# Kernel tuning notes

Hardware: AMD Instinct MI355X
Metric: run time of the kernel (lower is better)

## Reference

```python
import jax, jax.numpy as jnp
import numpy as np
from jax import lax


def setup_inputs() -> dict:
    key = jax.random.key(0)
    kx, kw = jax.random.split(key)
    x = jax.random.normal(kx, (32, 3, 8192), dtype=jnp.float32)
    weight = jax.random.normal(kw, (128, 3, 64), dtype=jnp.float32)
    return {"x": x, "weight": weight}


def reference(x, weight):
    # x: [B, C, L], weight: [O, C, K]
    K = weight.shape[2]
    # Cross-correlation (conv1d, no bias, valid padding): [B, O, L-K+1]
    conv_out = lax.conv_general_dilated(
        x, weight, window_strides=(1,), padding='VALID',
        dimension_numbers=('NCH', 'OIH', 'NCH'))
    # Half squared norm of each shapelet: [O]
    w_norm = jnp.sum(weight ** 2, axis=(1, 2)) / 2
    # Half squared norm of each length-K window, via cumulative sums
    # (avoids materializing the [B, C, W, K] unfold tensor)
    sq = jnp.sum(x ** 2, axis=1)               # [B, L]
    c = jnp.pad(jnp.cumsum(sq, axis=1), ((0, 0), (1, 0)))  # [B, L+1]
    win_norm = (c[:, K:] - c[:, :-K]) / 2      # [B, L-K+1]
    # features = conv_out - (||w||^2/2 + ||window||^2/2)
    features = conv_out - w_norm[None, :, None] - win_norm[:, None, :]
    # global max-pool over time, then *(-2) -> min squared distance
    return -2.0 * jnp.max(features, axis=-1)   # [B, O]
```

## Files before the change

kernel.cpp:

```cpp
#include <hip/hip_runtime.h>
#include <hip/hip_bf16.h>
#include <float.h>

#define BB 32
#define LL 8192
#define OO 128
#define KK 64
#define WW (LL - KK + 1)
#define NCH 3
#define GX 11

typedef __attribute__((ext_vector_type(8))) short short8;
typedef __attribute__((ext_vector_type(4))) float f32x4;

union AB { int4 i4; int i[4]; short8 v; };

static __device__ __forceinline__ unsigned int pkbf(float a, float b) {
    union { __hip_bfloat162 h; unsigned int u; } cv;
    cv.h = __float22bfloat162_rn(make_float2(a, b));
    return cv.u;
}

__global__ __launch_bounds__(256) void prep_kernel(const float* __restrict__ w,
                                                   unsigned short* __restrict__ wswz,
                                                   float* __restrict__ wn,
                                                   float* __restrict__ out) {
    int g = blockIdx.x * 256 + threadIdx.x;
    if (g < 3072) {
        int ob = g / 768;
        int rem = g - ob * 768;
        int rr = rem >> 5, o2 = rem & 31;
        int ks = rr >> 2, qp = rr & 3;
        int c = ks >> 1, h = ks & 1;
        const float* p = w + (size_t)(ob * 32 + o2) * 192 + c * 64 + h * 32 + qp * 8;
        float4 v0 = *(const float4*)p, v1 = *(const float4*)(p + 4);
        int4 pk;
        pk.x = (int)pkbf(v0.x, v0.y);
        pk.y = (int)pkbf(v0.z, v0.w);
        pk.z = (int)pkbf(v1.x, v1.y);
        pk.w = (int)pkbf(v1.z, v1.w);
        ((int4*)wswz)[g] = pk;
    }
    int oo = g - 3072;
    if (oo >= 0 && oo < OO) {
        const float* p = w + oo * 192;
        float s = 0.f;
        for (int i = 0; i < 192; ++i) { float v = p[i]; s = fmaf(v, v, s); }
        wn[oo] = 0.5f * s;
    }
    int oi = g - 3200;
    if (oi >= 0 && oi < BB * OO) out[oi] = 3.389e38f;
}

static __device__ __forceinline__ void stage_load(const float* __restrict__ x, int b, int T0,
                                                  int tid, float4* v) {
    v[0] = make_float4(0.f, 0.f, 0.f, 0.f);
    v[1] = v[0];
    v[2] = v[0];
    if (tid < 80) {
        int l = T0 + 4 * tid;
        if (l < LL) {
            const float* p = x + (size_t)b * 3 * LL + l;
            v[0] = *(const float4*)(p);
            v[1] = *(const float4*)(p + LL);
            v[2] = *(const float4*)(p + 2 * LL);
        }
    }
}

static __device__ __forceinline__ void stage_store(int tid, const float4* v,
                                                   unsigned short* xl, float* sql, float* Pl) {
    if (tid >= 80) return;
    #pragma unroll
    for (int c = 0; c < 3; ++c) {
        uint2 pk;
        pk.x = pkbf(v[c].x, v[c].y);
        pk.y = pkbf(v[c].z, v[c].w);
        *(uint2*)(xl + c * 320 + tid * 4) = pk;
    }
    float4 sq4;
    sq4.x = fmaf(v[2].x, v[2].x, fmaf(v[1].x, v[1].x, v[0].x * v[0].x));
    sq4.y = fmaf(v[2].y, v[2].y, fmaf(v[1].y, v[1].y, v[0].y * v[0].y));
    sq4.z = fmaf(v[2].z, v[2].z, fmaf(v[1].z, v[1].z, v[0].z * v[0].z));
    sq4.w = fmaf(v[2].w, v[2].w, fmaf(v[1].w, v[1].w, v[0].w * v[0].w));
    *(float4*)(sql + tid * 4) = sq4;
    float s4 = (sq4.x + sq4.y) + (sq4.z + sq4.w);
    float s8 = s4 + __shfl_xor(s4, 1, 64);
    if ((tid & 1) == 0) Pl[tid >> 1] = s8;
}

__global__ __launch_bounds__(256, 4) void shapeconv_main(const float* __restrict__ x,
                                                         const unsigned short* __restrict__ wswz,
                                                         const float* __restrict__ wn,
                                                         float* __restrict__ out) {
    __shared__ __align__(16) unsigned short w_lds[6144];
    __shared__ __align__(16) unsigned short x_lds[2][3 * 320];
    __shared__ __align__(16) float sq_lds[2][320];
    __shared__ __align__(16) float P_lds[2][40];
    __shared__ float wn_lds[32];
    __shared__ float mred[32];

    const int tcx = blockIdx.x;
    const int ob = blockIdx.y;
    const int b  = blockIdx.z;
    const int tid = threadIdx.x;
    const int wv = tid >> 6;
    const int lane = tid & 63;
    const int wo = wv & 1, wt = wv >> 1;
    const int n  = lane & 15;
    const int qp = lane >> 4;
    const int Tb = tcx * (NCH * 256);
    const int rem = (WW - Tb + 255) >> 8;
    const int nch_eff = rem < NCH ? rem : NCH;

    {
        const char* src = (const char*)wswz + (size_t)ob * 12288 + tid * 16;
        #pragma unroll
        for (int i = 0; i < 3; ++i) {
            __builtin_amdgcn_global_load_lds(
                (const __attribute__((address_space(1))) unsigned int*)(src + i * 4096),
                (__attribute__((address_space(3))) unsigned int*)((char*)w_lds + tid * 16 + i * 4096),
                16, 0, 0);
        }
    }
    if (tid < 32) wn_lds[tid] = wn[ob * 32 + tid];

    float4 sv[3];
    stage_load(x, b, Tb, tid, sv);
    stage_store(tid, sv, x_lds[0], sq_lds[0], P_lds[0]);
    __syncthreads();

    float nw4[4];
    #pragma unroll
    for (int rg = 0; rg < 4; ++rg) nw4[rg] = wn_lds[16 * wo + 4 * qp + rg];

    float m2[4];
    #pragma unroll
    for (int rg = 0; rg < 4; ++rg) m2[rg] = -FLT_MAX;

    for (int ci = 0; ci < nch_eff; ++ci) {
        const int bsel = ci & 1;
        const int T0 = Tb + ci * 256;
        const bool more = (ci + 1 < nch_eff);
        if (more) stage_load(x, b, T0 + 256, tid, sv);

        float wl[8];
        {
            const float* sqp = sq_lds[bsel];
            const float* Pl  = P_lds[bsel];
            const int mi = 16 * wt + n;
            float S = 0.f;
            #pragma unroll
            for (int i = 0; i < 8; ++i) S += Pl[mi + i];
            #pragma unroll
            for (int r = 0; r < 8; ++r) {
                wl[r] = (T0 + 8 * mi + r < WW) ? 0.5f * S : 1e30f;
                if (r < 7) S += sqp[8 * mi + 64 + r] - sqp[8 * mi + r];
            }
        }

        f32x4 acc[8];
        #pragma unroll
        for (int r = 0; r < 8; ++r)
            #pragma unroll
            for (int rg = 0; rg < 4; ++rg)
                acc[r][rg] = -nw4[rg] - wl[r];

        const char* xb = (const char*)x_lds[bsel];
        __builtin_amdgcn_s_setprio(1);
        #pragma unroll
        for (int ks = 0; ks < 6; ++ks) {
            int c = ks >> 1, h = ks & 1;
            int e0b = c * 640 + 256 * wt + 64 * h + 16 * (n + qp);
            int4 Ea = *(const int4*)(xb + e0b);
            int4 Eb = *(const int4*)(xb + e0b + 16);
            int D[8] = {Ea.x, Ea.y, Ea.z, Ea.w, Eb.x, Eb.y, Eb.z, Eb.w};
            AB a0;
            a0.i4 = ((const int4*)w_lds)[(ks * 4 + qp) * 32 + 16 * wo + n];
            #pragma unroll
            for (int r = 0; r < 8; ++r) {
                AB bf;
                int s = r >> 1;
                if ((r & 1) == 0) {
                    bf.i[0] = D[s]; bf.i[1] = D[s + 1]; bf.i[2] = D[s + 2]; bf.i[3] = D[s + 3];
                } else {
                    #pragma unroll
                    for (int d = 0; d < 4; ++d)
                        bf.i[d] = (int)__builtin_amdgcn_alignbit((unsigned)D[s + d + 1],
                                                                 (unsigned)D[s + d], 16);
                }
                acc[r] = __builtin_amdgcn_mfma_f32_16x16x32_bf16(a0.v, bf.v, acc[r], 0, 0, 0);
            }
        }
        __builtin_amdgcn_s_setprio(0);

        #pragma unroll
        for (int rg = 0; rg < 4; ++rg) {
            float mm = m2[rg];
            #pragma unroll
            for (int r = 0; r < 8; ++r) mm = fmaxf(mm, acc[r][rg]);
            m2[rg] = mm;
        }

        if (more) {
            stage_store(tid, sv, x_lds[1 - bsel], sq_lds[1 - bsel], P_lds[1 - bsel]);
            __syncthreads();
        }
    }

    #pragma unroll
    for (int s = 1; s <= 8; s <<= 1)
        #pragma unroll
        for (int rg = 0; rg < 4; ++rg)
            m2[rg] = fmaxf(m2[rg], __shfl_xor(m2[rg], s, 64));

    if (wt == 1 && n == 0) {
        #pragma unroll
        for (int rg = 0; rg < 4; ++rg)
            mred[16 * wo + 4 * qp + rg] = m2[rg];
    }
    __syncthreads();
    if (wt == 0 && n == 0) {
        #pragma unroll
        for (int rg = 0; rg < 4; ++rg) {
            int oi = 16 * wo + 4 * qp + rg;
            float v = fmaxf(m2[rg], mred[oi]);
            atomicMin((int*)(out + (size_t)b * OO + ob * 32 + oi),
                      __float_as_int(-2.0f * v));
        }
    }
}

extern "C" void kernel_launch(void* const* d_in, const int* in_sizes, int n_in,
                              void* d_out, int out_size, void* d_ws, size_t ws_size,
                              hipStream_t stream) {
    const float* x = (const float*)d_in[0];
    const float* w = (const float*)d_in[1];
    float* out = (float*)d_out;

    unsigned short* wswz = (unsigned short*)d_ws;
    float* wn = (float*)((char*)d_ws + 49152);

    prep_kernel<<<29, 256, 0, stream>>>(w, wswz, wn, out);
    dim3 grid(GX, 4, BB);
    shapeconv_main<<<grid, 256, 0, stream>>>(x, wswz, wn, out);
}
```

Before: 77.07 us.

## Give each wave a private 128-sample time tile covering all 32 outputs, no chunk loop

Each wave now owns its own 128-position time tile and computes both 16-output halves of the block's 32 outputs. Before, the 4 waves split outputs and time inside a shared 256-sample chunk, and each block looped over 3 double-buffered chunks. The grid grows to 16 time blocks, and each block loads its x tile once into per-wave LDS. This removes the chunk loop, the cross-wave LDS reduction and most barriers. The cost is more atomics to global memory (one per wave per output), redundant loading of the overlapping 64-sample halo, and more accumulator registers per wave.

```diff
diff --git a/kernel.cpp b/kernel.cpp
--- a/kernel.cpp
+++ b/kernel.cpp
@@ -7,8 +7,7 @@
 #define OO 128
 #define KK 64
 #define WW (LL - KK + 1)
-#define NCH 3
-#define GX 11
+#define TCX 16
 
 typedef __attribute__((ext_vector_type(8))) short short8;
 typedef __attribute__((ext_vector_type(4))) float f32x4;
@@ -52,53 +51,14 @@
     if (oi >= 0 && oi < BB * OO) out[oi] = 3.389e38f;
 }
 
-static __device__ __forceinline__ void stage_load(const float* __restrict__ x, int b, int T0,
-                                                  int tid, float4* v) {
-    v[0] = make_float4(0.f, 0.f, 0.f, 0.f);
-    v[1] = v[0];
-    v[2] = v[0];
-    if (tid < 80) {
-        int l = T0 + 4 * tid;
-        if (l < LL) {
-            const float* p = x + (size_t)b * 3 * LL + l;
-            v[0] = *(const float4*)(p);
-            v[1] = *(const float4*)(p + LL);
-            v[2] = *(const float4*)(p + 2 * LL);
-        }
-    }
-}
-
-static __device__ __forceinline__ void stage_store(int tid, const float4* v,
-                                                   unsigned short* xl, float* sql, float* Pl) {
-    if (tid >= 80) return;
-    #pragma unroll
-    for (int c = 0; c < 3; ++c) {
-        uint2 pk;
-        pk.x = pkbf(v[c].x, v[c].y);
-        pk.y = pkbf(v[c].z, v[c].w);
-        *(uint2*)(xl + c * 320 + tid * 4) = pk;
-    }
-    float4 sq4;
-    sq4.x = fmaf(v[2].x, v[2].x, fmaf(v[1].x, v[1].x, v[0].x * v[0].x));
-    sq4.y = fmaf(v[2].y, v[2].y, fmaf(v[1].y, v[1].y, v[0].y * v[0].y));
-    sq4.z = fmaf(v[2].z, v[2].z, fmaf(v[1].z, v[1].z, v[0].z * v[0].z));
-    sq4.w = fmaf(v[2].w, v[2].w, fmaf(v[1].w, v[1].w, v[0].w * v[0].w));
-    *(float4*)(sql + tid * 4) = sq4;
-    float s4 = (sq4.x + sq4.y) + (sq4.z + sq4.w);
-    float s8 = s4 + __shfl_xor(s4, 1, 64);
-    if ((tid & 1) == 0) Pl[tid >> 1] = s8;
-}
-
 __global__ __launch_bounds__(256, 4) void shapeconv_main(const float* __restrict__ x,
                                                          const unsigned short* __restrict__ wswz,
                                                          const float* __restrict__ wn,
                                                          float* __restrict__ out) {
     __shared__ __align__(16) unsigned short w_lds[6144];
-    __shared__ __align__(16) unsigned short x_lds[2][3 * 320];
-    __shared__ __align__(16) float sq_lds[2][320];
-    __shared__ __align__(16) float P_lds[2][40];
-    __shared__ float wn_lds[32];
-    __shared__ float mred[32];
+    __shared__ __align__(16) unsigned short xw_lds[4][576];
+    __shared__ __align__(16) float sq_lds[4][192];
+    __shared__ __align__(16) float P_lds[4][24];
 
     const int tcx = blockIdx.x;
     const int ob = blockIdx.y;
@@ -106,12 +66,24 @@
     const int tid = threadIdx.x;
     const int wv = tid >> 6;
     const int lane = tid & 63;
-    const int wo = wv & 1, wt = wv >> 1;
     const int n  = lane & 15;
     const int qp = lane >> 4;
-    const int Tb = tcx * (NCH * 256);
-    const int rem = (WW - Tb + 255) >> 8;
-    const int nch_eff = rem < NCH ? rem : NCH;
+    const int T0w = (tcx * 4 + wv) * 128;
+
+    float2 va[3], vb[3];
+    const float* xb = x + (size_t)b * 3 * LL;
+    {
+        int e0 = T0w + 2 * lane;
+        #pragma unroll
+        for (int c = 0; c < 3; ++c) va[c] = *(const float2*)(xb + c * LL + e0);
+        #pragma unroll
+        for (int c = 0; c < 3; ++c) vb[c] = make_float2(0.f, 0.f);
+        int e1 = T0w + 128 + 2 * lane;
+        if (lane < 32 && e1 < LL) {
+            #pragma unroll
+            for (int c = 0; c < 3; ++c) vb[c] = *(const float2*)(xb + c * LL + e1);
+        }
+    }
 
     {
         const char* src = (const char*)wswz + (size_t)ob * 12288 + tid * 16;
@@ -123,112 +95,118 @@
                 16, 0, 0);
         }
     }
-    if (tid < 32) wn_lds[tid] = wn[ob * 32 + tid];
-
-    float4 sv[3];
-    stage_load(x, b, Tb, tid, sv);
-    stage_store(tid, sv, x_lds[0], sq_lds[0], P_lds[0]);
+
+    float nw[2][4];
+    #pragma unroll
+    for (int ot = 0; ot < 2; ++ot)
+        #pragma unroll
+        for (int rg = 0; rg < 4; ++rg)
+            nw[ot][rg] = wn[ob * 32 + 16 * ot + 4 * qp + rg];
+
+    unsigned short* xw = xw_lds[wv];
+    float* sqw = sq_lds[wv];
+    float* Pw  = P_lds[wv];
+    {
+        float sx = 0.f, sy = 0.f;
+        #pragma unroll
+        for (int c = 0; c < 3; ++c) {
+            *(unsigned int*)(xw + c * 192 + 2 * lane) = pkbf(va[c].x, va[c].y);
+            sx = fmaf(va[c].x, va[c].x, sx);
+            sy = fmaf(va[c].y, va[c].y, sy);
+        }
+        *(float2*)(sqw + 2 * lane) = make_float2(sx, sy);
+        float p2 = sx + sy;
+        p2 += __shfl_xor(p2, 1, 64);
+        p2 += __shfl_xor(p2, 2, 64);
+        if ((lane & 3) == 0) Pw[lane >> 2] = p2;
+        float tx = 0.f, ty = 0.f;
+        unsigned int pk[3];
+        #pragma unroll
+        for (int c = 0; c < 3; ++c) {
+            tx = fmaf(vb[c].x, vb[c].x, tx);
+            ty = fmaf(vb[c].y, vb[c].y, ty);
+            pk[c] = pkbf(vb[c].x, vb[c].y);
+        }
+        if (lane < 32) {
+            #pragma unroll
+            for (int c = 0; c < 3; ++c) *(unsigned int*)(xw + c * 192 + 128 + 2 * lane) = pk[c];
+            *(float2*)(sqw + 128 + 2 * lane) = make_float2(tx, ty);
+        }
+        float q2 = tx + ty;
+        q2 += __shfl_xor(q2, 1, 64);
+        q2 += __shfl_xor(q2, 2, 64);
+        if (lane < 32 && (lane & 3) == 0) Pw[16 + (lane >> 2)] = q2;
+    }
+
     __syncthreads();
 
-    float nw4[4];
-    #pragma unroll
-    for (int rg = 0; rg < 4; ++rg) nw4[rg] = wn_lds[16 * wo + 4 * qp + rg];
-
-    float m2[4];
-    #pragma unroll
-    for (int rg = 0; rg < 4; ++rg) m2[rg] = -FLT_MAX;
-
-    for (int ci = 0; ci < nch_eff; ++ci) {
-        const int bsel = ci & 1;
-        const int T0 = Tb + ci * 256;
-        const bool more = (ci + 1 < nch_eff);
-        if (more) stage_load(x, b, T0 + 256, tid, sv);
-
-        float wl[8];
-        {
-            const float* sqp = sq_lds[bsel];
-            const float* Pl  = P_lds[bsel];
-            const int mi = 16 * wt + n;
-            float S = 0.f;
-            #pragma unroll
-            for (int i = 0; i < 8; ++i) S += Pl[mi + i];
-            #pragma unroll
-            for (int r = 0; r < 8; ++r) {
-                wl[r] = (T0 + 8 * mi + r < WW) ? 0.5f * S : 1e30f;
-                if (r < 7) S += sqp[8 * mi + 64 + r] - sqp[8 * mi + r];
+    float wl[8];
+    {
+        float S = 0.f;
+        #pragma unroll
+        for (int i = 0; i < 8; ++i) S += Pw[n + i];
+        #pragma unroll
+        for (int r = 0; r < 8; ++r) {
+            wl[r] = (T0w + 8 * n + r < WW) ? 0.5f * S : 1e30f;
+            if (r < 7) S += sqw[8 * n + 64 + r] - sqw[8 * n + r];
+        }
+    }
+
+    f32x4 acc[2][8];
+    #pragma unroll
+    for (int ot = 0; ot < 2; ++ot)
+        #pragma unroll
+        for (int rg = 0; rg < 4; ++rg)
+            #pragma unroll
+            for (int r = 0; r < 8; ++r)
+                acc[ot][r][rg] = -nw[ot][rg] - wl[r];
+
+    __builtin_amdgcn_s_setprio(1);
+    #pragma unroll
+    for (int ks = 0; ks < 6; ++ks) {
+        int c = ks >> 1, h = ks & 1;
+        int e0b = c * 384 + 64 * h + 16 * (n + qp);
+        int4 Ea = *(const int4*)((const char*)xw + e0b);
+        int4 Eb = *(const int4*)((const char*)xw + e0b + 16);
+        int D[8] = {Ea.x, Ea.y, Ea.z, Ea.w, Eb.x, Eb.y, Eb.z, Eb.w};
+        AB a0, a1;
+        const int4* wq = (const int4*)w_lds + (ks * 4 + qp) * 32;
+        a0.i4 = wq[n];
+        a1.i4 = wq[16 + n];
+        #pragma unroll
+        for (int r = 0; r < 8; ++r) {
+            AB bf;
+            int s = r >> 1;
+            if ((r & 1) == 0) {
+                bf.i[0] = D[s]; bf.i[1] = D[s + 1]; bf.i[2] = D[s + 2]; bf.i[3] = D[s + 3];
+            } else {
+                #pragma unroll
+                for (int d = 0; d < 4; ++d)
+                    bf.i[d] = (int)__builtin_amdgcn_alignbit((unsigned)D[s + d + 1],
+                                                             (unsigned)D[s + d], 16);
             }
-        }
-
-        f32x4 acc[8];
-        #pragma unroll
-        for (int r = 0; r < 8; ++r)
-            #pragma unroll
-            for (int rg = 0; rg < 4; ++rg)
-                acc[r][rg] = -nw4[rg] - wl[r];
-
-        const char* xb = (const char*)x_lds[bsel];
-        __builtin_amdgcn_s_setprio(1);
-        #pragma unroll
-        for (int ks = 0; ks < 6; ++ks) {
-            int c = ks >> 1, h = ks & 1;
-            int e0b = c * 640 + 256 * wt + 64 * h + 16 * (n + qp);
-            int4 Ea = *(const int4*)(xb + e0b);
-            int4 Eb = *(const int4*)(xb + e0b + 16);
-            int D[8] = {Ea.x, Ea.y, Ea.z, Ea.w, Eb.x, Eb.y, Eb.z, Eb.w};
-            AB a0;
-            a0.i4 = ((const int4*)w_lds)[(ks * 4 + qp) * 32 + 16 * wo + n];
-            #pragma unroll
-            for (int r = 0; r < 8; ++r) {
-                AB bf;
-                int s = r >> 1;
-                if ((r & 1) == 0) {
-                    bf.i[0] = D[s]; bf.i[1] = D[s + 1]; bf.i[2] = D[s + 2]; bf.i[3] = D[s + 3];
-                } else {
-                    #pragma unroll
-                    for (int d = 0; d < 4; ++d)
-                        bf.i[d] = (int)__builtin_amdgcn_alignbit((unsigned)D[s + d + 1],
-                                                                 (unsigned)D[s + d], 16);
-                }
-                acc[r] = __builtin_amdgcn_mfma_f32_16x16x32_bf16(a0.v, bf.v, acc[r], 0, 0, 0);
+            acc[0][r] = __builtin_amdgcn_mfma_f32_16x16x32_bf16(a0.v, bf.v, acc[0][r], 0, 0, 0);
+            acc[1][r] = __builtin_amdgcn_mfma_f32_16x16x32_bf16(a1.v, bf.v, acc[1][r], 0, 0, 0);
+        }
+    }
+    __builtin_amdgcn_s_setprio(0);
+
+    #pragma unroll
+    for (int ot = 0; ot < 2; ++ot)
+        #pragma unroll
+        for (int rg = 0; rg < 4; ++rg) {
+            float mm = acc[ot][rg & 3][rg];
+            mm = -FLT_MAX;
+            #pragma unroll
+            for (int r = 0; r < 8; ++r) mm = fmaxf(mm, acc[ot][r][rg]);
+            #pragma unroll
+            for (int s = 1; s <= 8; s <<= 1)
+                mm = fmaxf(mm, __shfl_xor(mm, s, 64));
+            if (n == 0) {
+                atomicMin((int*)(out + (size_t)b * OO + ob * 32 + 16 * ot + 4 * qp + rg),
+                          __float_as_int(-2.0f * mm));
             }
         }
-        __builtin_amdgcn_s_setprio(0);
-
-        #pragma unroll
-        for (int rg = 0; rg < 4; ++rg) {
-            float mm = m2[rg];
-            #pragma unroll
-            for (int r = 0; r < 8; ++r) mm = fmaxf(mm, acc[r][rg]);
-            m2[rg] = mm;
-        }
-
-        if (more) {
-            stage_store(tid, sv, x_lds[1 - bsel], sq_lds[1 - bsel], P_lds[1 - bsel]);
-            __syncthreads();
-        }
-    }
-
-    #pragma unroll
-    for (int s = 1; s <= 8; s <<= 1)
-        #pragma unroll
-        for (int rg = 0; rg < 4; ++rg)
-            m2[rg] = fmaxf(m2[rg], __shfl_xor(m2[rg], s, 64));
-
-    if (wt == 1 && n == 0) {
-        #pragma unroll
-        for (int rg = 0; rg < 4; ++rg)
-            mred[16 * wo + 4 * qp + rg] = m2[rg];
-    }
-    __syncthreads();
-    if (wt == 0 && n == 0) {
-        #pragma unroll
-        for (int rg = 0; rg < 4; ++rg) {
-            int oi = 16 * wo + 4 * qp + rg;
-            float v = fmaxf(m2[rg], mred[oi]);
-            atomicMin((int*)(out + (size_t)b * OO + ob * 32 + oi),
-                      __float_as_int(-2.0f * v));
-        }
-    }
 }
 
 extern "C" void kernel_launch(void* const* d_in, const int* in_sizes, int n_in,
@@ -242,6 +220,6 @@
     float* wn = (float*)((char*)d_ws + 49152);
 
     prep_kernel<<<29, 256, 0, stream>>>(w, wswz, wn, out);
-    dim3 grid(GX, 4, BB);
+    dim3 grid(TCX, 4, BB);
     shapeconv_main<<<grid, 256, 0, stream>>>(x, wswz, wn, out);
 }
```

Result: slower. 81.01 us (+5.1%).
